# Optimization experiments

Measured on AMD Instinct MI355X. Metric: run time of the kernel, lower is better.

## Reference

```python
import jax, jax.numpy as jnp
import numpy as np

D_H, HEAD, LAYER_IDX = 1024, 16, 11
D_ATTN = D_H // HEAD
BZ, LEN = 2, 2048


def setup_inputs() -> dict:
    key = jax.random.key(0)
    ks = jax.random.split(key, 8)
    s = 1.0 / np.sqrt(D_H)
    v = jax.random.normal(ks[0], (BZ, LEN, D_H), jnp.float32)
    k = jax.random.normal(ks[1], (BZ, LEN, D_H), jnp.float32)
    q = jax.random.normal(ks[2], (BZ, LEN, D_H), jnp.float32)
    # causal mask: 1.0 where attention is blocked (j > i)
    causal = jnp.triu(jnp.ones((LEN, LEN), jnp.float32), k=1)
    mask = jnp.broadcast_to(causal[None, None], (BZ, 1, LEN, LEN))
    Wv = jax.random.normal(ks[3], (D_H, D_H), jnp.float32) * s
    Wk = jax.random.normal(ks[4], (D_H, D_H), jnp.float32) * s
    Wq = jax.random.normal(ks[5], (D_H, D_H), jnp.float32) * s
    Wo = jax.random.normal(ks[6], (D_H, D_H), jnp.float32) * s
    bo = jnp.zeros((D_H,), jnp.float32)
    return {"v": v, "k": k, "q": q, "mask": mask,
            "Wv": Wv, "Wk": Wk, "Wq": Wq, "Wo": Wo, "bo": bo}


def _split_head(x):
    # (bz, len, d_h) -> (bz, head, len, d_attn)
    bz, L, _ = x.shape
    return x.reshape(bz, L, HEAD, D_ATTN).transpose(0, 2, 1, 3)


def reference(v, k, q, mask, Wv, Wk, Wq, Wo, bo):
    bz, len_q, _ = q.shape
    vh = _split_head(v @ Wv)  # (bz, head, len_k, d_attn)
    kh = _split_head(k @ Wk)
    qh = _split_head(q @ Wq)
    scale = 1.0 / jnp.sqrt(jnp.asarray(D_ATTN, jnp.float32))
    weight = jnp.einsum("bhqd,bhkd->bhqk", qh, kh) * scale
    weight = weight + mask * (-1e9)
    weight = weight / jnp.asarray(LAYER_IDX + 1, jnp.float32)
    attn = jax.nn.softmax(weight, axis=-1)  # dropout omitted (inference)
    out = jnp.einsum("bhqk,bhkd->bhqd", attn, vh)
    out = out.transpose(0, 2, 1, 3).reshape(bz, len_q, D_H)
    return out @ Wo + bo
```

## Files before the change

kernel.cpp:

```cpp
#include <hip/hip_runtime.h>
#include <hip/hip_fp16.h>

typedef _Float16 f16;
typedef _Float16 f16x4 __attribute__((ext_vector_type(4)));
typedef _Float16 f16x8 __attribute__((ext_vector_type(8)));
typedef float f32x4 __attribute__((ext_vector_type(4)));

#define D_H   1024
#define LEN   2048
#define BZ    2
#define NHEAD 16
#define DA    64
#define MTOK  (BZ * LEN)
#define KDIM  1024
#define ATT_SCALE (0.125f / 12.0f)

__device__ __forceinline__ void load_lds16(const f16* g, f16* l) {
  __builtin_amdgcn_global_load_lds((const __attribute__((address_space(1))) void*)g,
                                   (__attribute__((address_space(3))) void*)l,
                                   16, 0, 0);
}

#define FENCE() __asm__ volatile("" ::: "memory")

__global__ __launch_bounds__(256)
void k_prep(const float* __restrict__ W0, const float* __restrict__ W1,
            const float* __restrict__ W2, const float* __restrict__ W3,
            const float* __restrict__ xq, const float* __restrict__ xk,
            const float* __restrict__ xv,
            f16* __restrict__ T0, f16* __restrict__ T1,
            f16* __restrict__ T2, f16* __restrict__ T3,
            f16* __restrict__ q16, f16* __restrict__ k16,
            f16* __restrict__ v16) {
  const int z = blockIdx.z;
  const int tid = threadIdx.x;
  if (z < 4) {
    const float* W = (z == 0) ? W0 : (z == 1) ? W1 : (z == 2) ? W2 : W3;
    f16* Wt = (z == 0) ? T0 : (z == 1) ? T1 : (z == 2) ? T2 : T3;
    __shared__ float tile[64][68];
    const int r0 = blockIdx.y * 64, c0 = blockIdx.x * 64;
    {
      const int row = tid >> 2, cq = (tid & 3) * 16;
      const float* src = W + (size_t)(r0 + row) * D_H + c0 + cq;
      float4 v0 = *(const float4*)(src + 0);
      float4 v1 = *(const float4*)(src + 4);
      float4 v2 = *(const float4*)(src + 8);
      float4 v3 = *(const float4*)(src + 12);
      *(float4*)&tile[row][cq + 0]  = v0;
      *(float4*)&tile[row][cq + 4]  = v1;
      *(float4*)&tile[row][cq + 8]  = v2;
      *(float4*)&tile[row][cq + 12] = v3;
    }
    __syncthreads();
    {
      const int c = tid >> 2, rq = (tid & 3) * 16;
      f16 ov[16];
#pragma unroll
      for (int j = 0; j < 16; ++j) ov[j] = (f16)tile[rq + j][c];
      f16* dst = Wt + (size_t)(c0 + c) * D_H + r0 + rq;
      *(f16x8*)(dst + 0) = *(f16x8*)&ov[0];
      *(f16x8*)(dst + 8) = *(f16x8*)&ov[8];
    }
  } else {
    const float* in = (z == 4) ? xq : (z == 5) ? xk : xv;
    f16* out = (z == 4) ? q16 : (z == 5) ? k16 : v16;
    const size_t blk = ((size_t)(blockIdx.y * 16 + blockIdx.x)) * 16384;
#pragma unroll
    for (int s = 0; s < 16; ++s) {
      size_t off = blk + (size_t)(s * 256 + tid) * 4;
      float4 x = *(const float4*)(in + off);
      f16x4 o; o[0] = (f16)x.x; o[1] = (f16)x.y; o[2] = (f16)x.z; o[3] = (f16)x.w;
      *(f16x4*)(out + off) = o;
    }
  }
}

#define BM2 256
#define BN2 256
#define BKT 64
#define NKT (KDIM / BKT)

__global__ __launch_bounds__(512, 2)
void k_gemm3(const f16* __restrict__ A0, const f16* __restrict__ A1,
             const f16* __restrict__ A2, const f16* __restrict__ W0,
             const f16* __restrict__ W1, const f16* __restrict__ W2,
             f16* __restrict__ O0, f16* __restrict__ O1, f16* __restrict__ O2) {
  __shared__ __align__(16) f16 smem3[65536];
  f16* As = smem3;
  f16* Bs = smem3 + 32768;
  const int lin = blockIdx.x + 16 * blockIdx.y + 64 * blockIdx.z;
  const int w = (lin & 7) * 24 + (lin >> 3);
  const int z = w >> 6;
  const int rem = w & 63;
  const int m0 = (rem >> 2) * BM2, n0 = (rem & 3) * BN2;
  const f16* A = (z == 0) ? A0 : (z == 1) ? A1 : A2;
  const f16* Bt = (z == 0) ? W0 : (z == 1) ? W1 : W2;
  f16* Out = (z == 0) ? O0 : (z == 1) ? O1 : O2;
  const int tid = threadIdx.x;
  const int wave = tid >> 6, lane = tid & 63;
  const int lc = lane & 15, quad = lane >> 4;
  const int wr = wave >> 2, wc = wave & 3;
  const f16* Ab = A + (size_t)m0 * KDIM;
  const f16* Bb = Bt + (size_t)n0 * KDIM;

  f32x4 acc[8][4] = {};

#define STAGE_HALF(g, ldsbase, kt, h)                                         \
  {                                                                           \
    _Pragma("unroll")                                                         \
    for (int r = 0; r < 2; ++r) {                                             \
      int idx = tid + r * 512;                                                \
      int row = (h) * 128 + (idx >> 3);                                       \
      int gch = (idx & 7) ^ (row & 7);                                        \
      load_lds16((g) + (size_t)row * KDIM + (kt) * BKT + gch * 8,             \
                 (ldsbase) + (h) * 8192 + idx * 8);                           \
    }                                                                         \
  }

#define READ_A(mh, kc)                                                        \
  _Pragma("unroll")                                                           \
  for (int i = 0; i < 4; ++i) {                                               \
    int row = wr * 128 + ((mh) * 4 + i) * 16 + lc;                            \
    int pc = ((kc) * 4 + quad) ^ (row & 7);                                   \
    af[i] = *(const f16x8*)&Ad[row * 64 + pc * 8];                            \
  }
#define READ_B(kc)                                                            \
  _Pragma("unroll")                                                           \
  for (int n = 0; n < 4; ++n) {                                               \
    int row = wc * 64 + n * 16 + lc;                                          \
    int pc = ((kc) * 4 + quad) ^ (row & 7);                                   \
    bf[n] = *(const f16x8*)&Bd[row * 64 + pc * 8];                            \
  }
#define MFMA_Q(mh)                                                            \
  FENCE(); __builtin_amdgcn_s_barrier();                                      \
  __builtin_amdgcn_s_setprio(1);                                              \
  _Pragma("unroll")                                                           \
  for (int i = 0; i < 4; ++i)                                                 \
    _Pragma("unroll")                                                         \
    for (int n = 0; n < 4; ++n)                                               \
      acc[(mh) * 4 + i][n] = __builtin_amdgcn_mfma_f32_16x16x32_f16(          \
          af[i], bf[n], acc[(mh) * 4 + i][n], 0, 0, 0);                       \
  __builtin_amdgcn_s_setprio(0);                                              \
  __asm__ volatile("s_waitcnt lgkmcnt(0)" ::: "memory");                      \
  FENCE(); __builtin_amdgcn_s_barrier(); FENCE();

  STAGE_HALF(Ab, As, 0, 0);
  STAGE_HALF(Ab, As, 0, 1);
  STAGE_HALF(Bb, Bs, 0, 0);
  STAGE_HALF(Bb, Bs, 0, 1);
  STAGE_HALF(Ab, As + 16384, 1, 0);
  __asm__ volatile("s_waitcnt vmcnt(2)" ::: "memory");
  __builtin_amdgcn_s_barrier();
  FENCE();

  for (int t = 0; t < NKT; ++t) {
    const f16* Ad = As + (t & 1) * 16384;
    const f16* Bd = Bs + (t & 1) * 16384;
    f16* AdW = As + (t & 1) * 16384;
    f16* Adn = As + ((t + 1) & 1) * 16384;
    f16* Bdn = Bs + ((t + 1) & 1) * 16384;
    const bool pf = (t + 1 < NKT);
    f16x8 af[4], bf[4];

    READ_A(0, 0); READ_B(0);
    if (pf) STAGE_HALF(Ab, Adn, t + 1, 1);
    MFMA_Q(0);

    READ_A(1, 0);
    if (pf) STAGE_HALF(Bb, Bdn, t + 1, 0);
    MFMA_Q(1);

    READ_A(0, 1); READ_B(1);
    if (pf) STAGE_HALF(Bb, Bdn, t + 1, 1);
    MFMA_Q(0);

    READ_A(1, 1);
    FENCE(); __builtin_amdgcn_s_barrier();
    if (t + 2 < NKT) STAGE_HALF(Ab, AdW, t + 2, 0);
    __builtin_amdgcn_s_setprio(1);
#pragma unroll
    for (int i = 0; i < 4; ++i)
#pragma unroll
      for (int n = 0; n < 4; ++n)
        acc[4 + i][n] = __builtin_amdgcn_mfma_f32_16x16x32_f16(
            af[i], bf[n], acc[4 + i][n], 0, 0, 0);
    __builtin_amdgcn_s_setprio(0);
    if (t + 2 < NKT) {
      __asm__ volatile("s_waitcnt vmcnt(2)" ::: "memory");
    } else if (pf) {
      __asm__ volatile("s_waitcnt vmcnt(0)" ::: "memory");
    }
    __asm__ volatile("s_waitcnt lgkmcnt(0)" ::: "memory");
    FENCE(); __builtin_amdgcn_s_barrier(); FENCE();
  }

  if (z <= 1) {
    f16* slice = smem3 + wave * 8192;
#pragma unroll
    for (int mi = 0; mi < 8; ++mi)
#pragma unroll
      for (int ni = 0; ni < 4; ++ni)
#pragma unroll
        for (int rr = 0; rr < 4; ++rr) {
          int tl = mi * 16 + quad * 4 + rr;
          int d = ni * 16 + lc;
          slice[tl * 64 + (((d >> 3) ^ (tl & 7)) << 3) + (d & 7)] =
              (f16)acc[mi][ni][rr];
        }
    __asm__ volatile("s_waitcnt lgkmcnt(0)" ::: "memory");
    const int h = (n0 >> 6) + wc;
    const int tokbase = m0 + wr * 128;
    const int b = tokbase >> 11, ib = tokbase & 2047;
#pragma unroll
    for (int s = 0; s < 16; ++s) {
      int u = lane + s * 64;
      int tl = u >> 3, ch = u & 7;
      f16x8 vv = *(const f16x8*)&slice[tl * 64 + ((ch ^ (tl & 7)) << 3)];
      *(f16x8*)(Out + ((size_t)((b << 4) + h) * LEN + ib + tl) * DA + ch * 8) = vv;
    }
  } else {
    f16* Ct = smem3;
#pragma unroll
    for (int e = 0; e < 2; ++e) {
      __syncthreads();
      if (wr == e) {
#pragma unroll
        for (int mi = 0; mi < 8; ++mi)
#pragma unroll
          for (int ni = 0; ni < 4; ++ni)
#pragma unroll
            for (int rr = 0; rr < 4; ++rr) {
              int tl = mi * 16 + quad * 4 + rr;
              int dl = wc * 64 + ni * 16 + lc;
              Ct[dl * 136 + tl] = (f16)acc[mi][ni][rr];
            }
      }
      __syncthreads();
      const int tokbase = m0 + e * 128;
      const int b = tokbase >> 11, j0 = tokbase & 2047;
#pragma unroll
      for (int s = 0; s < 8; ++s) {
        int u = tid + s * 512;
        int dl = u >> 4, ch = u & 15;
        f16x8 vv = *(const f16x8*)&Ct[dl * 136 + ch * 8];
        *(f16x8*)(Out + ((size_t)(b * 1024 + n0 + dl)) * LEN + j0 + ch * 8) = vv;
      }
    }
  }
}

#define OM 64
#define ON 128
#define BK 64
#define ONIT (KDIM / BK)
__global__ __launch_bounds__(256)
void k_gemm_out(const f16* __restrict__ A, const f16* __restrict__ Bt,
                float* __restrict__ Out, const float* __restrict__ bias) {
  __shared__ __align__(16) char smem[2 * (OM + ON) * BK * 2];
  f16* As = (f16*)smem;
  f16* Bs = As + 2 * OM * BK;
  const int m0 = blockIdx.x * OM, n0 = blockIdx.y * ON;
  const int tid = threadIdx.x;
  const int wave = tid >> 6, lane = tid & 63;
  const int lc = lane & 15, quad = lane >> 4;
  const int wm = (wave >> 1) * 32, wn = (wave & 1) * 64;
  const int swz = lc & 7;
  const f16* Abase = A + (size_t)m0 * KDIM;
  const f16* Bbase = Bt + (size_t)n0 * KDIM;

  f32x4 acc[2][4] = {};

#define STAGE_OUT(t)                                                          \
  {                                                                           \
    int k0s = (t) * BK;                                                       \
    f16* Ad = As + ((t) & 1) * (OM * BK);                                     \
    f16* Bd = Bs + ((t) & 1) * (ON * BK);                                     \
    _Pragma("unroll")                                                         \
    for (int r = 0; r < 2; ++r) {                                             \
      int idx = tid + r * 256;                                                \
      int row = idx >> 3, ch = idx & 7;                                       \
      int gch = ch ^ (row & 7);                                               \
      load_lds16(Abase + (size_t)row * KDIM + k0s + gch * 8, &Ad[idx * 8]);   \
    }                                                                         \
    _Pragma("unroll")                                                         \
    for (int r = 0; r < 4; ++r) {                                             \
      int idx = tid + r * 256;                                                \
      int row = idx >> 3, ch = idx & 7;                                       \
      int gch = ch ^ (row & 7);                                               \
      load_lds16(Bbase + (size_t)row * KDIM + k0s + gch * 8, &Bd[idx * 8]);   \
    }                                                                         \
  }

  STAGE_OUT(0);
  for (int t = 0; t < ONIT; ++t) {
    __syncthreads();
    if (t + 1 < ONIT) STAGE_OUT(t + 1);
    const f16* Ad = As + (t & 1) * (OM * BK);
    const f16* Bd = Bs + (t & 1) * (ON * BK);
    __builtin_amdgcn_s_setprio(1);
#pragma unroll
    for (int kc = 0; kc < 2; ++kc) {
      f16x8 af[2], bf[4];
#pragma unroll
      for (int mi = 0; mi < 2; ++mi)
        af[mi] = *(const f16x8*)&Ad[(wm + mi * 16 + lc) * 64 +
                                    (((kc * 4 + quad) ^ swz) * 8)];
#pragma unroll
      for (int ni = 0; ni < 4; ++ni)
        bf[ni] = *(const f16x8*)&Bd[(wn + ni * 16 + lc) * 64 +
                                    (((kc * 4 + quad) ^ swz) * 8)];
#pragma unroll
      for (int mi = 0; mi < 2; ++mi)
#pragma unroll
        for (int ni = 0; ni < 4; ++ni)
          acc[mi][ni] = __builtin_amdgcn_mfma_f32_16x16x32_f16(
              af[mi], bf[ni], acc[mi][ni], 0, 0, 0);
    }
    __builtin_amdgcn_s_setprio(0);
  }

  float* Ct = (float*)smem;
#pragma unroll
  for (int hf = 0; hf < 2; ++hf) {
    __syncthreads();
    if ((wave & 1) == hf) {
#pragma unroll
      for (int mi = 0; mi < 2; ++mi)
#pragma unroll
        for (int ni = 0; ni < 4; ++ni)
#pragma unroll
          for (int r = 0; r < 4; ++r) {
            int tok = wm + mi * 16 + quad * 4 + r;
            int d = ni * 16 + lc;
            Ct[tok * 68 + d] = acc[mi][ni][r];
          }
    }
    __syncthreads();
#pragma unroll
    for (int it = 0; it < 4; ++it) {
      int u = tid + it * 256;
      int tok = u >> 4, ch = u & 15;
      int gm = m0 + tok;
      int gc = n0 + hf * 64 + ch * 4;
      float4 bv = *(const float4*)(bias + gc);
      float4 cv = *(const float4*)&Ct[tok * 68 + ch * 4];
      float4 ov;
      ov.x = cv.x + bv.x; ov.y = cv.y + bv.y;
      ov.z = cv.z + bv.z; ov.w = cv.w + bv.w;
      *(float4*)(Out + (size_t)gm * D_H + gc) = ov;
    }
  }
}

__global__ __launch_bounds__(512, 4)
void k_attn(const f16* __restrict__ Qh, const f16* __restrict__ Kh,
            const f16* __restrict__ Vt, f16* __restrict__ O16) {
  __shared__ f16 Ks[2][64 * 64];
  __shared__ f16 Vs[2][64 * 64];
  __shared__ f16 Pw[8][16 * 64];
  const int tid = threadIdx.x;
  const int wave = tid >> 6, lane = tid & 63;
  const int lc = lane & 15, quad = lane >> 4;
  const int swz = lc & 7;
  const int bh = blockIdx.x & 31;
  const int idx16 = blockIdx.x >> 5;
  const int qb = (idx16 < 8) ? (15 - idx16) : (idx16 - 8);
  const int i0 = qb * 128 + wave * 16;
  const int b = bh >> 4, h = bh & 15;
  const f16* Qb = Qh + (size_t)bh * LEN * DA;
  const f16* Kb = Kh + (size_t)bh * LEN * DA;
  const f16* Vb = Vt + (size_t)bh * DA * LEN;

  f16x8 aQ[2];
  const f16 qs = (f16)ATT_SCALE;
#pragma unroll
  for (int c = 0; c < 2; ++c) {
    aQ[c] = *(const f16x8*)(Qb + (size_t)(i0 + lc) * DA + c * 32 + quad * 8);
#pragma unroll
    for (int j = 0; j < 8; ++j) aQ[c][j] = aQ[c][j] * qs;
  }

  float lsum = 0.f;
  f32x4 accO[4] = {};
  f16* P = &Pw[wave][0];

  const int niter = 2 * qb + 2;

  {
    int row = tid >> 3, ch = tid & 7;
    int gch = ch ^ (row & 7);
    load_lds16(Kb + (size_t)row * DA + gch * 8, &Ks[0][tid * 8]);
    load_lds16(Vb + (size_t)row * LEN + gch * 8, &Vs[0][tid * 8]);
  }

  for (int t = 0; t < niter; ++t) {
    __syncthreads();
    if (t + 1 < niter) {
      int j0n = (t + 1) * 64, nb = (t + 1) & 1;
      int row = tid >> 3, ch = tid & 7;
      int gch = ch ^ (row & 7);
      load_lds16(Kb + (size_t)(j0n + row) * DA + gch * 8, &Ks[nb][tid * 8]);
      load_lds16(Vb + (size_t)row * LEN + j0n + gch * 8, &Vs[nb][tid * 8]);
    }
    const f16* ks = Ks[t & 1];
    const f16* vs = Vs[t & 1];

    f32x4 st[4] = {};
    __builtin_amdgcn_s_setprio(1);
#pragma unroll
    for (int g = 0; g < 4; ++g)
#pragma unroll
      for (int c = 0; c < 2; ++c) {
        f16x8 aK = *(const f16x8*)&ks[(g * 16 + lc) * 64 +
                                      (((c * 4 + quad) ^ swz) * 8)];
        st[g] = __builtin_amdgcn_mfma_f32_16x16x32_f16(aK, aQ[c], st[g], 0, 0, 0);
      }
    __builtin_amdgcn_s_setprio(0);
    float ev[4][4];
    if (t >= niter - 2) {
      const int j0 = t * 64, q = i0 + lc;
#pragma unroll
      for (int g = 0; g < 4; ++g)
#pragma unroll
        for (int r = 0; r < 4; ++r) {
          int key = j0 + g * 16 + quad * 4 + r;
          float e = __expf(st[g][r]);
          e = (key > q) ? 0.f : e;
          lsum += e;
          ev[g][r] = e;
        }
    } else {
#pragma unroll
      for (int g = 0; g < 4; ++g)
#pragma unroll
        for (int r = 0; r < 4; ++r) {
          float e = __expf(st[g][r]);
          lsum += e;
          ev[g][r] = e;
        }
    }
#pragma unroll
    for (int g = 0; g < 4; ++g) {
      int c8 = ((g << 1) + (quad >> 1)) ^ swz;
      f16x4 pk;
      pk[0] = (f16)ev[g][0]; pk[1] = (f16)ev[g][1];
      pk[2] = (f16)ev[g][2]; pk[3] = (f16)ev[g][3];
      *(f16x4*)&P[lc * 64 + c8 * 8 + (quad & 1) * 4] = pk;
    }
    __asm__ volatile("s_waitcnt lgkmcnt(0)" ::: "memory");
    f16x8 aP[2];
#pragma unroll
    for (int c = 0; c < 2; ++c) {
      int c8 = (quad + 4 * c) ^ swz;
      aP[c] = *(const f16x8*)&P[lc * 64 + c8 * 8];
    }
    __builtin_amdgcn_s_setprio(1);
#pragma unroll
    for (int dc = 0; dc < 4; ++dc) {
      f16x8 bV0 = *(const f16x8*)&vs[(dc * 16 + lc) * 64 + ((quad ^ swz) * 8)];
      f16x8 bV1 = *(const f16x8*)&vs[(dc * 16 + lc) * 64 + (((4 + quad) ^ swz) * 8)];
      accO[dc] = __builtin_amdgcn_mfma_f32_16x16x32_f16(aP[0], bV0, accO[dc], 0, 0, 0);
      accO[dc] = __builtin_amdgcn_mfma_f32_16x16x32_f16(aP[1], bV1, accO[dc], 0, 0, 0);
    }
    __builtin_amdgcn_s_setprio(0);
  }

  lsum += __shfl_xor(lsum, 16, 64);
  lsum += __shfl_xor(lsum, 32, 64);
  float ls[4];
#pragma unroll
  for (int r = 0; r < 4; ++r) ls[r] = __shfl(lsum, quad * 4 + r, 64);

#pragma unroll
  for (int dc = 0; dc < 4; ++dc)
#pragma unroll
    for (int r = 0; r < 4; ++r) {
      int i = i0 + quad * 4 + r;
      int d = dc * 16 + lc;
      float v = accO[dc][r] / ls[r];
      O16[((size_t)(b * LEN + i)) * D_H + h * DA + d] = (f16)v;
    }
}

extern "C" void kernel_launch(void* const* d_in, const int* in_sizes, int n_in,
                              void* d_out, int out_size, void* d_ws, size_t ws_size,
                              hipStream_t stream) {
  const float* v_f = (const float*)d_in[0];
  const float* k_f = (const float*)d_in[1];
  const float* q_f = (const float*)d_in[2];
  const float* Wv = (const float*)d_in[4];
  const float* Wk = (const float*)d_in[5];
  const float* Wq = (const float*)d_in[6];
  const float* Wo = (const float*)d_in[7];
  const float* bo = (const float*)d_in[8];
  float* out = (float*)d_out;

  const size_t SZ_X = (size_t)MTOK * D_H;
  const size_t SZ_W = (size_t)D_H * D_H;
  f16* ws = (f16*)d_ws;
  f16* q16 = ws;
  f16* k16 = ws + SZ_X;
  f16* v16 = ws + 2 * SZ_X;
  f16* Qh  = ws + 3 * SZ_X;
  f16* Kh  = ws + 4 * SZ_X;
  f16* Vt  = ws + 5 * SZ_X;
  f16* Wqt = ws + 6 * SZ_X;
  f16* Wkt = Wqt + SZ_W;
  f16* Wvt = Wqt + 2 * SZ_W;
  f16* Wot = Wqt + 3 * SZ_W;
  f16* O16 = q16;

  k_prep<<<dim3(16, 16, 7), 256, 0, stream>>>(
      Wq, Wk, Wv, Wo, q_f, k_f, v_f, Wqt, Wkt, Wvt, Wot, q16, k16, v16);

  k_gemm3<<<dim3(MTOK / BM2, D_H / BN2, 3), 512, 0, stream>>>(
      q16, k16, v16, Wqt, Wkt, Wvt, Qh, Kh, Vt);

  k_attn<<<dim3(32 * 16), 512, 0, stream>>>(Qh, Kh, Vt, O16);

  k_gemm_out<<<dim3(MTOK / OM, D_H / ON), 256, 0, stream>>>(O16, Wot, out, bo);
}
```

Measured before the change: 222.4 us.

## Restructure causal attention into paired 64-row query blocks per 4-wave workgroup

The attention kernel now uses 256-thread workgroups with 64-row query blocks. Each workgroup processes two blocks in sequence, a late one (31-pr) and an early one (pr), so every workgroup gets the same amount of causal work. Because of the smaller query tile, only the final key tile needs masking, which removes wasted fully-masked tiles. The softmax scale is folded with log2(e) so it can use exp2f, and the row-sum is computed as a tree. The cost is that each K/V tile is reused by half as many query rows, and the two segments run serially within a block.

```diff
diff --git a/kernel.cpp b/kernel.cpp
--- a/kernel.cpp
+++ b/kernel.cpp
@@ -352,134 +352,158 @@
   }
 }
 
-__global__ __launch_bounds__(512, 4)
+__global__ __launch_bounds__(256, 2)
 void k_attn(const f16* __restrict__ Qh, const f16* __restrict__ Kh,
             const f16* __restrict__ Vt, f16* __restrict__ O16) {
   __shared__ f16 Ks[2][64 * 64];
   __shared__ f16 Vs[2][64 * 64];
-  __shared__ f16 Pw[8][16 * 64];
+  __shared__ f16 Pw[4][16 * 64];
   const int tid = threadIdx.x;
   const int wave = tid >> 6, lane = tid & 63;
   const int lc = lane & 15, quad = lane >> 4;
   const int swz = lc & 7;
   const int bh = blockIdx.x & 31;
-  const int idx16 = blockIdx.x >> 5;
-  const int qb = (idx16 < 8) ? (15 - idx16) : (idx16 - 8);
-  const int i0 = qb * 128 + wave * 16;
+  const int pr = blockIdx.x >> 5;
   const int b = bh >> 4, h = bh & 15;
   const f16* Qb = Qh + (size_t)bh * LEN * DA;
   const f16* Kb = Kh + (size_t)bh * LEN * DA;
   const f16* Vb = Vt + (size_t)bh * DA * LEN;
-
-  f16x8 aQ[2];
-  const f16 qs = (f16)ATT_SCALE;
-#pragma unroll
-  for (int c = 0; c < 2; ++c) {
-    aQ[c] = *(const f16x8*)(Qb + (size_t)(i0 + lc) * DA + c * 32 + quad * 8);
-#pragma unroll
-    for (int j = 0; j < 8; ++j) aQ[c][j] = aQ[c][j] * qs;
-  }
-
-  float lsum = 0.f;
-  f32x4 accO[4] = {};
   f16* P = &Pw[wave][0];
-
-  const int niter = 2 * qb + 2;
-
-  {
-    int row = tid >> 3, ch = tid & 7;
-    int gch = ch ^ (row & 7);
-    load_lds16(Kb + (size_t)row * DA + gch * 8, &Ks[0][tid * 8]);
-    load_lds16(Vb + (size_t)row * LEN + gch * 8, &Vs[0][tid * 8]);
-  }
-
-  for (int t = 0; t < niter; ++t) {
+  const f16 qs = (f16)(ATT_SCALE * 1.44269504088896340736f);
+
+#pragma unroll
+  for (int seg = 0; seg < 2; ++seg) {
+    const int qb = seg ? pr : 31 - pr;
+    const int i0 = qb * 64 + wave * 16;
+    const int niter = qb + 1;
+
+    f16x8 aQ[2];
+#pragma unroll
+    for (int c = 0; c < 2; ++c) {
+      aQ[c] = *(const f16x8*)(Qb + (size_t)(i0 + lc) * DA + c * 32 + quad * 8);
+#pragma unroll
+      for (int j = 0; j < 8; ++j) aQ[c][j] = aQ[c][j] * qs;
+    }
+    float lsum = 0.f;
+    f32x4 accO[4] = {};
+
     __syncthreads();
-    if (t + 1 < niter) {
-      int j0n = (t + 1) * 64, nb = (t + 1) & 1;
-      int row = tid >> 3, ch = tid & 7;
+#pragma unroll
+    for (int r = 0; r < 2; ++r) {
+      int idx = tid + r * 256;
+      int row = idx >> 3, ch = idx & 7;
       int gch = ch ^ (row & 7);
-      load_lds16(Kb + (size_t)(j0n + row) * DA + gch * 8, &Ks[nb][tid * 8]);
-      load_lds16(Vb + (size_t)row * LEN + j0n + gch * 8, &Vs[nb][tid * 8]);
-    }
-    const f16* ks = Ks[t & 1];
-    const f16* vs = Vs[t & 1];
-
-    f32x4 st[4] = {};
-    __builtin_amdgcn_s_setprio(1);
-#pragma unroll
-    for (int g = 0; g < 4; ++g)
+      load_lds16(Kb + (size_t)row * DA + gch * 8, &Ks[0][idx * 8]);
+    }
+#pragma unroll
+    for (int r = 0; r < 2; ++r) {
+      int idx = tid + r * 256;
+      int row = idx >> 3, ch = idx & 7;
+      int gch = ch ^ (row & 7);
+      load_lds16(Vb + (size_t)row * LEN + gch * 8, &Vs[0][idx * 8]);
+    }
+
+    for (int t = 0; t < niter; ++t) {
+      __syncthreads();
+      if (t + 1 < niter) {
+        int j0n = (t + 1) * 64, nb = (t + 1) & 1;
+#pragma unroll
+        for (int r = 0; r < 2; ++r) {
+          int idx = tid + r * 256;
+          int row = idx >> 3, ch = idx & 7;
+          int gch = ch ^ (row & 7);
+          load_lds16(Kb + (size_t)(j0n + row) * DA + gch * 8, &Ks[nb][idx * 8]);
+        }
+#pragma unroll
+        for (int r = 0; r < 2; ++r) {
+          int idx = tid + r * 256;
+          int row = idx >> 3, ch = idx & 7;
+          int gch = ch ^ (row & 7);
+          load_lds16(Vb + (size_t)row * LEN + j0n + gch * 8, &Vs[nb][idx * 8]);
+        }
+      }
+      const f16* ks = Ks[t & 1];
+      const f16* vs = Vs[t & 1];
+
+      f32x4 st[4] = {};
+      __builtin_amdgcn_s_setprio(1);
+#pragma unroll
+      for (int g = 0; g < 4; ++g)
+#pragma unroll
+        for (int c = 0; c < 2; ++c) {
+          f16x8 aK = *(const f16x8*)&ks[(g * 16 + lc) * 64 +
+                                        (((c * 4 + quad) ^ swz) * 8)];
+          st[g] = __builtin_amdgcn_mfma_f32_16x16x32_f16(aK, aQ[c], st[g], 0, 0, 0);
+        }
+      __builtin_amdgcn_s_setprio(0);
+
+      float ev[4][4];
+      if (t == niter - 1) {
+        const int j0 = t * 64, q = i0 + lc;
+#pragma unroll
+        for (int g = 0; g < 4; ++g)
+#pragma unroll
+          for (int r = 0; r < 4; ++r) {
+            int key = j0 + g * 16 + quad * 4 + r;
+            float e = exp2f(st[g][r]);
+            e = (key > q) ? 0.f : e;
+            ev[g][r] = e;
+          }
+      } else {
+#pragma unroll
+        for (int g = 0; g < 4; ++g)
+#pragma unroll
+          for (int r = 0; r < 4; ++r) ev[g][r] = exp2f(st[g][r]);
+      }
+      {
+        float g0 = (ev[0][0] + ev[0][1]) + (ev[0][2] + ev[0][3]);
+        float g1 = (ev[1][0] + ev[1][1]) + (ev[1][2] + ev[1][3]);
+        float g2 = (ev[2][0] + ev[2][1]) + (ev[2][2] + ev[2][3]);
+        float g3 = (ev[3][0] + ev[3][1]) + (ev[3][2] + ev[3][3]);
+        lsum += (g0 + g1) + (g2 + g3);
+      }
+#pragma unroll
+      for (int g = 0; g < 4; ++g) {
+        int c8 = ((g << 1) + (quad >> 1)) ^ swz;
+        f16x4 pk;
+        pk[0] = (f16)ev[g][0]; pk[1] = (f16)ev[g][1];
+        pk[2] = (f16)ev[g][2]; pk[3] = (f16)ev[g][3];
+        *(f16x4*)&P[lc * 64 + c8 * 8 + (quad & 1) * 4] = pk;
+      }
+      __asm__ volatile("s_waitcnt lgkmcnt(0)" ::: "memory");
+      f16x8 aP[2];
 #pragma unroll
       for (int c = 0; c < 2; ++c) {
-        f16x8 aK = *(const f16x8*)&ks[(g * 16 + lc) * 64 +
-                                      (((c * 4 + quad) ^ swz) * 8)];
-        st[g] = __builtin_amdgcn_mfma_f32_16x16x32_f16(aK, aQ[c], st[g], 0, 0, 0);
-      }
-    __builtin_amdgcn_s_setprio(0);
-    float ev[4][4];
-    if (t >= niter - 2) {
-      const int j0 = t * 64, q = i0 + lc;
-#pragma unroll
-      for (int g = 0; g < 4; ++g)
-#pragma unroll
-        for (int r = 0; r < 4; ++r) {
-          int key = j0 + g * 16 + quad * 4 + r;
-          float e = __expf(st[g][r]);
-          e = (key > q) ? 0.f : e;
-          lsum += e;
-          ev[g][r] = e;
-        }
-    } else {
-#pragma unroll
-      for (int g = 0; g < 4; ++g)
-#pragma unroll
-        for (int r = 0; r < 4; ++r) {
-          float e = __expf(st[g][r]);
-          lsum += e;
-          ev[g][r] = e;
-        }
-    }
-#pragma unroll
-    for (int g = 0; g < 4; ++g) {
-      int c8 = ((g << 1) + (quad >> 1)) ^ swz;
-      f16x4 pk;
-      pk[0] = (f16)ev[g][0]; pk[1] = (f16)ev[g][1];
-      pk[2] = (f16)ev[g][2]; pk[3] = (f16)ev[g][3];
-      *(f16x4*)&P[lc * 64 + c8 * 8 + (quad & 1) * 4] = pk;
-    }
-    __asm__ volatile("s_waitcnt lgkmcnt(0)" ::: "memory");
-    f16x8 aP[2];
-#pragma unroll
-    for (int c = 0; c < 2; ++c) {
-      int c8 = (quad + 4 * c) ^ swz;
-      aP[c] = *(const f16x8*)&P[lc * 64 + c8 * 8];
-    }
-    __builtin_amdgcn_s_setprio(1);
-#pragma unroll
-    for (int dc = 0; dc < 4; ++dc) {
-      f16x8 bV0 = *(const f16x8*)&vs[(dc * 16 + lc) * 64 + ((quad ^ swz) * 8)];
-      f16x8 bV1 = *(const f16x8*)&vs[(dc * 16 + lc) * 64 + (((4 + quad) ^ swz) * 8)];
-      accO[dc] = __builtin_amdgcn_mfma_f32_16x16x32_f16(aP[0], bV0, accO[dc], 0, 0, 0);
-      accO[dc] = __builtin_amdgcn_mfma_f32_16x16x32_f16(aP[1], bV1, accO[dc], 0, 0, 0);
-    }
-    __builtin_amdgcn_s_setprio(0);
-  }
-
-  lsum += __shfl_xor(lsum, 16, 64);
-  lsum += __shfl_xor(lsum, 32, 64);
-  float ls[4];
-#pragma unroll
-  for (int r = 0; r < 4; ++r) ls[r] = __shfl(lsum, quad * 4 + r, 64);
-
-#pragma unroll
-  for (int dc = 0; dc < 4; ++dc)
-#pragma unroll
-    for (int r = 0; r < 4; ++r) {
-      int i = i0 + quad * 4 + r;
-      int d = dc * 16 + lc;
-      float v = accO[dc][r] / ls[r];
-      O16[((size_t)(b * LEN + i)) * D_H + h * DA + d] = (f16)v;
-    }
+        int c8 = (quad + 4 * c) ^ swz;
+        aP[c] = *(const f16x8*)&P[lc * 64 + c8 * 8];
+      }
+      __builtin_amdgcn_s_setprio(1);
+#pragma unroll
+      for (int dc = 0; dc < 4; ++dc) {
+        f16x8 bV0 = *(const f16x8*)&vs[(dc * 16 + lc) * 64 + ((quad ^ swz) * 8)];
+        f16x8 bV1 = *(const f16x8*)&vs[(dc * 16 + lc) * 64 + (((4 + quad) ^ swz) * 8)];
+        accO[dc] = __builtin_amdgcn_mfma_f32_16x16x32_f16(aP[0], bV0, accO[dc], 0, 0, 0);
+        accO[dc] = __builtin_amdgcn_mfma_f32_16x16x32_f16(aP[1], bV1, accO[dc], 0, 0, 0);
+      }
+      __builtin_amdgcn_s_setprio(0);
+    }
+
+    lsum += __shfl_xor(lsum, 16, 64);
+    lsum += __shfl_xor(lsum, 32, 64);
+    float ls[4];
+#pragma unroll
+    for (int r = 0; r < 4; ++r) ls[r] = __shfl(lsum, quad * 4 + r, 64);
+
+#pragma unroll
+    for (int dc = 0; dc < 4; ++dc)
+#pragma unroll
+      for (int r = 0; r < 4; ++r) {
+        int i = i0 + quad * 4 + r;
+        int d = dc * 16 + lc;
+        float v = accO[dc][r] / ls[r];
+        O16[((size_t)(b * LEN + i)) * D_H + h * DA + d] = (f16)v;
+      }
+  }
 }
 
 extern "C" void kernel_launch(void* const* d_in, const int* in_sizes, int n_in,
@@ -516,7 +540,7 @@
   k_gemm3<<<dim3(MTOK / BM2, D_H / BN2, 3), 512, 0, stream>>>(
       q16, k16, v16, Wqt, Wkt, Wvt, Qh, Kh, Vt);
 
-  k_attn<<<dim3(32 * 16), 512, 0, stream>>>(Qh, Kh, Vt, O16);
+  k_attn<<<dim3(32 * 16), 256, 0, stream>>>(Qh, Kh, Vt, O16);
 
   k_gemm_out<<<dim3(MTOK / OM, D_H / ON), 256, 0, stream>>>(O16, Wot, out, bo);
 }
```

Result: no change. 222.2 us (-0.1%).

## Rewrite attention as per-wave 32-query tiles with register-only K/V and 32x32 MFMA

Applied to the files above, without the earlier changes.

The attention kernel now gives each wave its own 32-query block, loading K and V fragments straight from global memory into registers with double buffering, so it no longer needs LDS staging or block-level barriers. It uses 32x32x16 MFMAs and rebuilds the P operand through cross-half lane shuffles instead of writing P to LDS and reading it back. It also folds log2(e) into the Q scale so it can use exp2f. The trade-off is that waves sharing a head no longer share K/V through LDS, which increases global/L2 traffic, and register pressure goes up.

```diff
diff --git a/kernel.cpp b/kernel.cpp
--- a/kernel.cpp
+++ b/kernel.cpp
@@ -5,6 +5,7 @@
 typedef _Float16 f16x4 __attribute__((ext_vector_type(4)));
 typedef _Float16 f16x8 __attribute__((ext_vector_type(8)));
 typedef float f32x4 __attribute__((ext_vector_type(4)));
+typedef float f32x16 __attribute__((ext_vector_type(16)));
 
 #define D_H   1024
 #define LEN   2048
@@ -22,6 +23,12 @@
 }
 
 #define FENCE() __asm__ volatile("" ::: "memory")
+
+__device__ __forceinline__ unsigned pk2(float a, float b) {
+  union { f16 h; unsigned short u; } ca, cb;
+  ca.h = (f16)a; cb.h = (f16)b;
+  return (unsigned)ca.u | ((unsigned)cb.u << 16);
+}
 
 __global__ __launch_bounds__(256)
 void k_prep(const float* __restrict__ W0, const float* __restrict__ W1,
@@ -352,134 +359,111 @@
   }
 }
 
-__global__ __launch_bounds__(512, 4)
+__global__ __launch_bounds__(256, 2)
 void k_attn(const f16* __restrict__ Qh, const f16* __restrict__ Kh,
             const f16* __restrict__ Vt, f16* __restrict__ O16) {
-  __shared__ f16 Ks[2][64 * 64];
-  __shared__ f16 Vs[2][64 * 64];
-  __shared__ f16 Pw[8][16 * 64];
   const int tid = threadIdx.x;
-  const int wave = tid >> 6, lane = tid & 63;
-  const int lc = lane & 15, quad = lane >> 4;
-  const int swz = lc & 7;
-  const int bh = blockIdx.x & 31;
-  const int idx16 = blockIdx.x >> 5;
-  const int qb = (idx16 < 8) ? (15 - idx16) : (idx16 - 8);
-  const int i0 = qb * 128 + wave * 16;
+  const int wid = blockIdx.x * 4 + (tid >> 6);
+  const int lane = tid & 63;
+  const int cq = lane & 31, half = lane >> 5;
+  const int jb = (wid < 1024) ? (63 - (wid >> 5)) : ((wid - 1024) >> 5);
+  const int bh = wid & 31;
   const int b = bh >> 4, h = bh & 15;
   const f16* Qb = Qh + (size_t)bh * LEN * DA;
   const f16* Kb = Kh + (size_t)bh * LEN * DA;
   const f16* Vb = Vt + (size_t)bh * DA * LEN;
-
-  f16x8 aQ[2];
-  const f16 qs = (f16)ATT_SCALE;
-#pragma unroll
-  for (int c = 0; c < 2; ++c) {
-    aQ[c] = *(const f16x8*)(Qb + (size_t)(i0 + lc) * DA + c * 32 + quad * 8);
-#pragma unroll
-    for (int j = 0; j < 8; ++j) aQ[c][j] = aQ[c][j] * qs;
-  }
-
+  const f16 qs = (f16)(ATT_SCALE * 1.44269504088896340736f);
+
+  f16x8 qf[4];
+#pragma unroll
+  for (int d = 0; d < 4; ++d) {
+    qf[d] = *(const f16x8*)(Qb + (size_t)(jb * 32 + cq) * DA + d * 16 + half * 8);
+#pragma unroll
+    for (int j = 0; j < 8; ++j) qf[d][j] = qf[d][j] * qs;
+  }
+
+  f32x16 acc0 = {}, acc1 = {};
   float lsum = 0.f;
-  f32x4 accO[4] = {};
-  f16* P = &Pw[wave][0];
-
-  const int niter = 2 * qb + 2;
-
-  {
-    int row = tid >> 3, ch = tid & 7;
-    int gch = ch ^ (row & 7);
-    load_lds16(Kb + (size_t)row * DA + gch * 8, &Ks[0][tid * 8]);
-    load_lds16(Vb + (size_t)row * LEN + gch * 8, &Vs[0][tid * 8]);
-  }
-
-  for (int t = 0; t < niter; ++t) {
-    __syncthreads();
-    if (t + 1 < niter) {
-      int j0n = (t + 1) * 64, nb = (t + 1) & 1;
-      int row = tid >> 3, ch = tid & 7;
-      int gch = ch ^ (row & 7);
-      load_lds16(Kb + (size_t)(j0n + row) * DA + gch * 8, &Ks[nb][tid * 8]);
-      load_lds16(Vb + (size_t)row * LEN + j0n + gch * 8, &Vs[nb][tid * 8]);
-    }
-    const f16* ks = Ks[t & 1];
-    const f16* vs = Vs[t & 1];
-
-    f32x4 st[4] = {};
-    __builtin_amdgcn_s_setprio(1);
-#pragma unroll
-    for (int g = 0; g < 4; ++g)
-#pragma unroll
-      for (int c = 0; c < 2; ++c) {
-        f16x8 aK = *(const f16x8*)&ks[(g * 16 + lc) * 64 +
-                                      (((c * 4 + quad) ^ swz) * 8)];
-        st[g] = __builtin_amdgcn_mfma_f32_16x16x32_f16(aK, aQ[c], st[g], 0, 0, 0);
-      }
-    __builtin_amdgcn_s_setprio(0);
-    float ev[4][4];
-    if (t >= niter - 2) {
-      const int j0 = t * 64, q = i0 + lc;
-#pragma unroll
-      for (int g = 0; g < 4; ++g)
-#pragma unroll
-        for (int r = 0; r < 4; ++r) {
-          int key = j0 + g * 16 + quad * 4 + r;
-          float e = __expf(st[g][r]);
-          e = (key > q) ? 0.f : e;
-          lsum += e;
-          ev[g][r] = e;
-        }
-    } else {
-#pragma unroll
-      for (int g = 0; g < 4; ++g)
-#pragma unroll
-        for (int r = 0; r < 4; ++r) {
-          float e = __expf(st[g][r]);
-          lsum += e;
-          ev[g][r] = e;
-        }
-    }
-#pragma unroll
-    for (int g = 0; g < 4; ++g) {
-      int c8 = ((g << 1) + (quad >> 1)) ^ swz;
-      f16x4 pk;
-      pk[0] = (f16)ev[g][0]; pk[1] = (f16)ev[g][1];
-      pk[2] = (f16)ev[g][2]; pk[3] = (f16)ev[g][3];
-      *(f16x4*)&P[lc * 64 + c8 * 8 + (quad & 1) * 4] = pk;
-    }
-    __asm__ volatile("s_waitcnt lgkmcnt(0)" ::: "memory");
-    f16x8 aP[2];
-#pragma unroll
-    for (int c = 0; c < 2; ++c) {
-      int c8 = (quad + 4 * c) ^ swz;
-      aP[c] = *(const f16x8*)&P[lc * 64 + c8 * 8];
-    }
-    __builtin_amdgcn_s_setprio(1);
-#pragma unroll
-    for (int dc = 0; dc < 4; ++dc) {
-      f16x8 bV0 = *(const f16x8*)&vs[(dc * 16 + lc) * 64 + ((quad ^ swz) * 8)];
-      f16x8 bV1 = *(const f16x8*)&vs[(dc * 16 + lc) * 64 + (((4 + quad) ^ swz) * 8)];
-      accO[dc] = __builtin_amdgcn_mfma_f32_16x16x32_f16(aP[0], bV0, accO[dc], 0, 0, 0);
-      accO[dc] = __builtin_amdgcn_mfma_f32_16x16x32_f16(aP[1], bV1, accO[dc], 0, 0, 0);
-    }
-    __builtin_amdgcn_s_setprio(0);
-  }
-
-  lsum += __shfl_xor(lsum, 16, 64);
+
+#define AT_LOAD(tt, KF, VF)                                                   \
+  {                                                                           \
+    const f16* kp = Kb + (size_t)((tt) * 32 + cq) * DA + half * 8;            \
+    KF[0] = *(const f16x8*)(kp);                                              \
+    KF[1] = *(const f16x8*)(kp + 16);                                         \
+    KF[2] = *(const f16x8*)(kp + 32);                                         \
+    KF[3] = *(const f16x8*)(kp + 48);                                         \
+    const f16* vp0 = Vb + (size_t)cq * LEN + (tt) * 32 + half * 8;            \
+    const f16* vp1 = Vb + (size_t)(32 + cq) * LEN + (tt) * 32 + half * 8;     \
+    VF[0] = *(const f16x8*)(vp0);                                             \
+    VF[1] = *(const f16x8*)(vp1);                                             \
+    VF[2] = *(const f16x8*)(vp0 + 16);                                        \
+    VF[3] = *(const f16x8*)(vp1 + 16);                                        \
+  }
+
+#define AT_COMPUTE(tt, KF, VF)                                                \
+  {                                                                           \
+    f32x16 st = {};                                                           \
+    st = __builtin_amdgcn_mfma_f32_32x32x16_f16(KF[0], qf[0], st, 0, 0, 0);   \
+    st = __builtin_amdgcn_mfma_f32_32x32x16_f16(KF[1], qf[1], st, 0, 0, 0);   \
+    st = __builtin_amdgcn_mfma_f32_32x32x16_f16(KF[2], qf[2], st, 0, 0, 0);   \
+    st = __builtin_amdgcn_mfma_f32_32x32x16_f16(KF[3], qf[3], st, 0, 0, 0);   \
+    float ev[16];                                                             \
+    if ((tt) == jb) {                                                         \
+      _Pragma("unroll")                                                       \
+      for (int r = 0; r < 16; ++r) {                                          \
+        int kl = (r & 3) + 8 * (r >> 2) + 4 * half;                           \
+        float e = exp2f(st[r]);                                               \
+        ev[r] = (kl > cq) ? 0.f : e;                                          \
+      }                                                                       \
+    } else {                                                                  \
+      _Pragma("unroll")                                                       \
+      for (int r = 0; r < 16; ++r) ev[r] = exp2f(st[r]);                      \
+    }                                                                         \
+    lsum += (((ev[0] + ev[1]) + (ev[2] + ev[3])) +                            \
+             ((ev[4] + ev[5]) + (ev[6] + ev[7]))) +                           \
+            (((ev[8] + ev[9]) + (ev[10] + ev[11])) +                          \
+             ((ev[12] + ev[13]) + (ev[14] + ev[15])));                        \
+    unsigned w0 = pk2(ev[0], ev[1]),  w1 = pk2(ev[2], ev[3]);                 \
+    unsigned w2 = pk2(ev[4], ev[5]),  w3 = pk2(ev[6], ev[7]);                 \
+    unsigned w4 = pk2(ev[8], ev[9]),  w5 = pk2(ev[10], ev[11]);               \
+    unsigned w6 = pk2(ev[12], ev[13]), w7 = pk2(ev[14], ev[15]);              \
+    unsigned p0 = __shfl_xor((int)w0, 32, 64), p1 = __shfl_xor((int)w1, 32, 64);\
+    unsigned p2 = __shfl_xor((int)w2, 32, 64), p3 = __shfl_xor((int)w3, 32, 64);\
+    unsigned p4 = __shfl_xor((int)w4, 32, 64), p5 = __shfl_xor((int)w5, 32, 64);\
+    unsigned p6 = __shfl_xor((int)w6, 32, 64), p7 = __shfl_xor((int)w7, 32, 64);\
+    union { unsigned u[4]; f16x8 v; } A0, A1;                                 \
+    A0.u[0] = half ? p2 : w0;  A0.u[1] = half ? p3 : w1;                      \
+    A0.u[2] = half ? w2 : p0;  A0.u[3] = half ? w3 : p1;                      \
+    A1.u[0] = half ? p6 : w4;  A1.u[1] = half ? p7 : w5;                      \
+    A1.u[2] = half ? w6 : p4;  A1.u[3] = half ? w7 : p5;                      \
+    acc0 = __builtin_amdgcn_mfma_f32_32x32x16_f16(A0.v, VF[0], acc0, 0, 0, 0);\
+    acc1 = __builtin_amdgcn_mfma_f32_32x32x16_f16(A0.v, VF[1], acc1, 0, 0, 0);\
+    acc0 = __builtin_amdgcn_mfma_f32_32x32x16_f16(A1.v, VF[2], acc0, 0, 0, 0);\
+    acc1 = __builtin_amdgcn_mfma_f32_32x32x16_f16(A1.v, VF[3], acc1, 0, 0, 0);\
+  }
+
+  f16x8 kfA[4], vfA[4], kfB[4], vfB[4];
+  const int niter = jb + 1;
+  AT_LOAD(0, kfA, vfA);
+  int t = 0;
+  for (; t + 1 < niter; t += 2) {
+    AT_LOAD(t + 1, kfB, vfB);
+    AT_COMPUTE(t, kfA, vfA);
+    if (t + 2 < niter) AT_LOAD(t + 2, kfA, vfA);
+    AT_COMPUTE(t + 1, kfB, vfB);
+  }
+  if (t < niter) AT_COMPUTE(t, kfA, vfA);
+
   lsum += __shfl_xor(lsum, 32, 64);
-  float ls[4];
-#pragma unroll
-  for (int r = 0; r < 4; ++r) ls[r] = __shfl(lsum, quad * 4 + r, 64);
-
-#pragma unroll
-  for (int dc = 0; dc < 4; ++dc)
-#pragma unroll
-    for (int r = 0; r < 4; ++r) {
-      int i = i0 + quad * 4 + r;
-      int d = dc * 16 + lc;
-      float v = accO[dc][r] / ls[r];
-      O16[((size_t)(b * LEN + i)) * D_H + h * DA + d] = (f16)v;
-    }
+  const size_t obase = ((size_t)b * LEN + jb * 32) * D_H + h * DA;
+#pragma unroll
+  for (int r = 0; r < 16; ++r) {
+    int rq = (r & 3) + 8 * (r >> 2) + 4 * half;
+    float ls = __shfl(lsum, rq, 64);
+    float inv = 1.0f / ls;
+    O16[obase + (size_t)rq * D_H + cq] = (f16)(acc0[r] * inv);
+    O16[obase + (size_t)rq * D_H + 32 + cq] = (f16)(acc1[r] * inv);
+  }
 }
 
 extern "C" void kernel_launch(void* const* d_in, const int* in_sizes, int n_in,
@@ -516,7 +500,7 @@
   k_gemm3<<<dim3(MTOK / BM2, D_H / BN2, 3), 512, 0, stream>>>(
       q16, k16, v16, Wqt, Wkt, Wvt, Qh, Kh, Vt);
 
-  k_attn<<<dim3(32 * 16), 512, 0, stream>>>(Qh, Kh, Vt, O16);
+  k_attn<<<dim3(512), 256, 0, stream>>>(Qh, Kh, Vt, O16);
 
   k_gemm_out<<<dim3(MTOK / OM, D_H / ON), 256, 0, stream>>>(O16, Wot, out, bo);
 }
```

After: 244.0 us. 1.1x slower.
